# Performance work log

Hardware: AMD Instinct MI355X
Metric: run time of the kernel (lower is better)

## Reference

```python
import math
import jax, jax.numpy as jnp
import numpy as np

IN_DIM, OUT_DIM, NUM_BASIS = 128, 64, 8
EPS = 1e-5

def _periods():
    # periods[i,j,g] = i*(out_dim*num_basis) + j*num_basis + g + 2
    i = jnp.arange(OUT_DIM)[:, None, None]
    j = jnp.arange(OUT_DIM)[None, :, None]
    g = jnp.arange(NUM_BASIS)[None, None, :]
    return (i * (OUT_DIM * NUM_BASIS) + j * NUM_BASIS + g + 2).astype(jnp.float32)

def setup_inputs() -> dict:
    key = jax.random.key(0)
    k1, k2, k3, k4 = jax.random.split(key, 4)
    x = jax.random.normal(k1, (2, 512, IN_DIM), dtype=jnp.float32)
    positions = jnp.arange(512, dtype=jnp.int32)
    M = jax.random.uniform(k2, (OUT_DIM, IN_DIM), minval=-0.5, maxval=0.5, dtype=jnp.float32)
    P = jax.random.uniform(k3, (OUT_DIM, OUT_DIM, NUM_BASIS), minval=-0.1, maxval=0.1, dtype=jnp.float32)
    gamma = jnp.ones((OUT_DIM,), dtype=jnp.float32)
    beta = jnp.zeros((OUT_DIM,), dtype=jnp.float32)
    Wres = jax.random.uniform(k4, (OUT_DIM, IN_DIM), minval=-0.1, maxval=0.1, dtype=jnp.float32)
    return {"x": x, "positions": positions, "M": M, "P": P, "gamma": gamma, "beta": beta, "Wres": Wres}

def reference(x, positions, M, P, gamma, beta, Wres):
    # x: (b, s, in), M: (out, in)
    x_trans = jnp.einsum('bsc,oc->bso', x, M)
    mu = jnp.mean(x_trans, axis=-1, keepdims=True)
    var = jnp.mean(jnp.square(x_trans - mu), axis=-1, keepdims=True)
    x_trans = (x_trans - mu) * jax.lax.rsqrt(var + EPS) * gamma + beta
    # phi[s,i,j,g] = cos(2*pi*k_s / periods[i,j,g])
    k = positions.astype(jnp.float32)[:, None, None, None]
    phi = jnp.cos(2.0 * math.pi * k / _periods())  # (s, out, out, nb)
    # Nk[b,s,i] = sum_{j,g} P[i,j,g] * x_trans[b,s,j] * phi[s,i,j,g]
    W = jnp.einsum('sijg,ijg->sij', phi, P)  # (s, out, out)
    Nk = jnp.einsum('bsj,sij->bsi', x_trans, W)
    residual = jnp.einsum('bsc,oc->bso', x, Wres)  # separate residual proj (in!=out)
    return Nk + residual
```

## Files before the change

kernel.cpp:

```cpp
#include <hip/hip_runtime.h>
#include <hip/hip_bf16.h>

#define IN_DIM    128
#define OUT_DIM   64
#define NUM_BASIS 8
#define SEQ       512
#define BATCH     2
#define EPS       1e-5f
#define SX        2

__global__ __launch_bounds__(512) void fused_layerts_kernel(
    const float* __restrict__ x,
    const float* __restrict__ M,
    const float* __restrict__ Wres,
    const float* __restrict__ gamma,
    const float* __restrict__ beta,
    const float* __restrict__ P,
    const int*   __restrict__ positions,
    float* __restrict__ out)
{
    const int s0  = blockIdx.x * SX;
    const int tid = threadIdx.x;

    __shared__ float xs [SX][BATCH][IN_DIM];
    __shared__ float xts[SX][BATCH][OUT_DIM];
    __shared__ float rs [SX][BATCH][OUT_DIM];
    __shared__ float pm [2][SX * BATCH][OUT_DIM];
    __shared__ float pr [2][SX * BATCH][OUT_DIM];
    __shared__ float part[8][SX][BATCH][OUT_DIM];

    {
        const int row = tid >> 7;
        const int c   = tid & 127;
        const int b   = row & 1;
        const int sl  = row >> 1;
        xs[sl][b][c] = x[((size_t)b * SEQ + (s0 + sl)) * IN_DIM + c];
    }
    const float k0 = (float)positions[s0];
    const float k1 = (float)positions[s0 + 1];
    __syncthreads();

    {
        const int o    = tid & 63;
        const int r    = (tid >> 6) & 3;
        const int half = tid >> 8;
        const int b    = r & 1;
        const int sl   = r >> 1;

        const float4* x4 = reinterpret_cast<const float4*>(&xs[sl][b][half * 64]);
        const float4* m4 = reinterpret_cast<const float4*>(M    + (size_t)o * IN_DIM + half * 64);
        const float4* w4 = reinterpret_cast<const float4*>(Wres + (size_t)o * IN_DIM + half * 64);

        float macc0 = 0.f, macc1 = 0.f, racc0 = 0.f, racc1 = 0.f;
#pragma unroll
        for (int c = 0; c < 16; c += 2) {
            float4 xv0 = x4[c],     mv0 = m4[c],     wv0 = w4[c];
            float4 xv1 = x4[c + 1], mv1 = m4[c + 1], wv1 = w4[c + 1];
            macc0 += xv0.x * mv0.x + xv0.y * mv0.y + xv0.z * mv0.z + xv0.w * mv0.w;
            racc0 += xv0.x * wv0.x + xv0.y * wv0.y + xv0.z * wv0.z + xv0.w * wv0.w;
            macc1 += xv1.x * mv1.x + xv1.y * mv1.y + xv1.z * mv1.z + xv1.w * mv1.w;
            racc1 += xv1.x * wv1.x + xv1.y * wv1.y + xv1.z * wv1.z + xv1.w * wv1.w;
        }
        pm[half][r][o] = macc0 + macc1;
        pr[half][r][o] = racc0 + racc1;
    }
    __syncthreads();

    if (tid < SX * BATCH * OUT_DIM) {
        const int o  = tid & 63;
        const int r  = tid >> 6;
        const int b  = r & 1;
        const int sl = r >> 1;

        const float macc = pm[0][r][o] + pm[1][r][o];
        const float racc = pr[0][r][o] + pr[1][r][o];

        float ssum = macc;
#pragma unroll
        for (int off = 32; off > 0; off >>= 1) ssum += __shfl_xor(ssum, off);
        const float mu = ssum * (1.0f / OUT_DIM);

        const float d = macc - mu;
        float v = d * d;
#pragma unroll
        for (int off = 32; off > 0; off >>= 1) v += __shfl_xor(v, off);
        const float var = v * (1.0f / OUT_DIM);

        xts[sl][b][o] = d * rsqrtf(var + EPS) * gamma[o] + beta[o];
        rs [sl][b][o] = racc;
    }
    __syncthreads();

    const int i   = tid & 63;
    const int grp = tid >> 6;

    float nk00 = 0.f, nk01 = 0.f, nk10 = 0.f, nk11 = 0.f;

#pragma unroll
    for (int jj = 0; jj < 8; ++jj) {
        const int j    = grp * 8 + jj;
        const int base = (i * OUT_DIM + j) * NUM_BASIS;
        const float4* Pp = reinterpret_cast<const float4*>(P + base);
        const float4 p0 = Pp[0];
        const float4 p1 = Pp[1];
        const float basef = (float)(base + 2);

        const float pv[8] = {p0.x, p0.y, p0.z, p0.w, p1.x, p1.y, p1.z, p1.w};
        float w0 = 0.f, w1 = 0.f;
#pragma unroll
        for (int g = 0; g < NUM_BASIS; ++g) {
            const float period = basef + (float)g;
            const float inv = __builtin_amdgcn_rcpf(period);
            float t0 = __builtin_amdgcn_fractf(k0 * inv);
            float t1 = __builtin_amdgcn_fractf(k1 * inv);
            w0 += pv[g] * __builtin_amdgcn_cosf(t0);
            w1 += pv[g] * __builtin_amdgcn_cosf(t1);
        }
        nk00 += xts[0][0][j] * w0;
        nk01 += xts[0][1][j] * w0;
        nk10 += xts[1][0][j] * w1;
        nk11 += xts[1][1][j] * w1;
    }

    part[grp][0][0][i] = nk00;
    part[grp][0][1][i] = nk01;
    part[grp][1][0][i] = nk10;
    part[grp][1][1][i] = nk11;
    __syncthreads();

    if (tid < SX * BATCH * OUT_DIM) {
        const int o  = tid & 63;
        const int r  = tid >> 6;
        const int b  = r & 1;
        const int sl = r >> 1;

        float sum = 0.f;
#pragma unroll
        for (int gg = 0; gg < 8; ++gg) sum += part[gg][sl][b][o];

        const size_t idx = ((size_t)b * SEQ + (s0 + sl)) * OUT_DIM + o;
        out[idx] = sum + rs[sl][b][o];
    }
}

extern "C" void kernel_launch(void* const* d_in, const int* in_sizes, int n_in,
                              void* d_out, int out_size, void* d_ws, size_t ws_size,
                              hipStream_t stream)
{
    const float* x         = (const float*)d_in[0];
    const int*   positions = (const int*)d_in[1];
    const float* M         = (const float*)d_in[2];
    const float* P         = (const float*)d_in[3];
    const float* gamma     = (const float*)d_in[4];
    const float* beta      = (const float*)d_in[5];
    const float* Wres      = (const float*)d_in[6];
    float* out = (float*)d_out;

    hipLaunchKernelGGL(fused_layerts_kernel, dim3(SEQ / SX), dim3(512), 0, stream,
                       x, M, Wres, gamma, beta, P, positions, out);
}
```

Before: 18.13 us.

## Warp-specialize: overlap projection/layernorm waves with cosine basis waves via LDS flag

Splits the block into two groups of four waves. The first group computes the input projection, residual and layernorm directly from global memory, with no shared staging and no split-K. The second group computes the cosine-weighted W rows (16 j each) at the same time, then spins on a workgroup-scope atomic flag before combining with the normalized activations. This removes three block-wide barriers and overlaps the transcendental work with the GEMV. In exchange, each cosine wave does twice the work, holds more registers, and spin-waits.

```diff
diff --git a/kernel.cpp b/kernel.cpp
--- a/kernel.cpp
+++ b/kernel.cpp
@@ -19,61 +19,45 @@
     const int*   __restrict__ positions,
     float* __restrict__ out)
 {
-    const int s0  = blockIdx.x * SX;
-    const int tid = threadIdx.x;
+    const int s0   = blockIdx.x * SX;
+    const int tid  = threadIdx.x;
+    const int lane = tid & 63;
+    const int wv   = tid >> 6;
 
-    __shared__ float xs [SX][BATCH][IN_DIM];
     __shared__ float xts[SX][BATCH][OUT_DIM];
     __shared__ float rs [SX][BATCH][OUT_DIM];
-    __shared__ float pm [2][SX * BATCH][OUT_DIM];
-    __shared__ float pr [2][SX * BATCH][OUT_DIM];
-    __shared__ float part[8][SX][BATCH][OUT_DIM];
+    __shared__ float part[4][SX][BATCH][OUT_DIM];
+    __shared__ int   ready;
 
-    {
-        const int row = tid >> 7;
-        const int c   = tid & 127;
-        const int b   = row & 1;
-        const int sl  = row >> 1;
-        xs[sl][b][c] = x[((size_t)b * SEQ + (s0 + sl)) * IN_DIM + c];
-    }
+    if (tid == 0) ready = 0;
+    __syncthreads();
+
     const float k0 = (float)positions[s0];
     const float k1 = (float)positions[s0 + 1];
-    __syncthreads();
 
-    {
-        const int o    = tid & 63;
-        const int r    = (tid >> 6) & 3;
-        const int half = tid >> 8;
-        const int b    = r & 1;
-        const int sl   = r >> 1;
+    if (wv < 4) {
+        const int r  = wv;
+        const int b  = r & 1;
+        const int sl = r >> 1;
+        const int o  = lane;
 
-        const float4* x4 = reinterpret_cast<const float4*>(&xs[sl][b][half * 64]);
-        const float4* m4 = reinterpret_cast<const float4*>(M    + (size_t)o * IN_DIM + half * 64);
-        const float4* w4 = reinterpret_cast<const float4*>(Wres + (size_t)o * IN_DIM + half * 64);
+        const float4* x4 = reinterpret_cast<const float4*>(
+            x + ((size_t)b * SEQ + (s0 + sl)) * IN_DIM);
+        const float4* m4 = reinterpret_cast<const float4*>(M    + (size_t)o * IN_DIM);
+        const float4* w4 = reinterpret_cast<const float4*>(Wres + (size_t)o * IN_DIM);
 
-        float macc0 = 0.f, macc1 = 0.f, racc0 = 0.f, racc1 = 0.f;
+        float ma = 0.f, mb = 0.f, ra = 0.f, rb = 0.f;
 #pragma unroll
-        for (int c = 0; c < 16; c += 2) {
+        for (int c = 0; c < 32; c += 2) {
             float4 xv0 = x4[c],     mv0 = m4[c],     wv0 = w4[c];
             float4 xv1 = x4[c + 1], mv1 = m4[c + 1], wv1 = w4[c + 1];
-            macc0 += xv0.x * mv0.x + xv0.y * mv0.y + xv0.z * mv0.z + xv0.w * mv0.w;
-            racc0 += xv0.x * wv0.x + xv0.y * wv0.y + xv0.z * wv0.z + xv0.w * wv0.w;
-            macc1 += xv1.x * mv1.x + xv1.y * mv1.y + xv1.z * mv1.z + xv1.w * mv1.w;
-            racc1 += xv1.x * wv1.x + xv1.y * wv1.y + xv1.z * wv1.z + xv1.w * wv1.w;
+            ma += xv0.x * mv0.x + xv0.y * mv0.y + xv0.z * mv0.z + xv0.w * mv0.w;
+            ra += xv0.x * wv0.x + xv0.y * wv0.y + xv0.z * wv0.z + xv0.w * wv0.w;
+            mb += xv1.x * mv1.x + xv1.y * mv1.y + xv1.z * mv1.z + xv1.w * mv1.w;
+            rb += xv1.x * wv1.x + xv1.y * wv1.y + xv1.z * wv1.z + xv1.w * wv1.w;
         }
-        pm[half][r][o] = macc0 + macc1;
-        pr[half][r][o] = racc0 + racc1;
-    }
-    __syncthreads();
-
-    if (tid < SX * BATCH * OUT_DIM) {
-        const int o  = tid & 63;
-        const int r  = tid >> 6;
-        const int b  = r & 1;
-        const int sl = r >> 1;
-
-        const float macc = pm[0][r][o] + pm[1][r][o];
-        const float racc = pr[0][r][o] + pr[1][r][o];
+        const float macc = ma + mb;
+        const float racc = ra + rb;
 
         float ssum = macc;
 #pragma unroll
@@ -88,44 +72,57 @@
 
         xts[sl][b][o] = d * rsqrtf(var + EPS) * gamma[o] + beta[o];
         rs [sl][b][o] = racc;
-    }
-    __syncthreads();
 
-    const int i   = tid & 63;
-    const int grp = tid >> 6;
+        __threadfence_block();
+        if (lane == 0)
+            __hip_atomic_fetch_add(&ready, 1, __ATOMIC_RELEASE,
+                                   __HIP_MEMORY_SCOPE_WORKGROUP);
+    } else {
+        const int g = wv - 4;
+        const int i = lane;
 
-    float nk00 = 0.f, nk01 = 0.f, nk10 = 0.f, nk11 = 0.f;
+        float w0[16], w1[16];
+#pragma unroll
+        for (int jj = 0; jj < 16; ++jj) {
+            const int j    = g * 16 + jj;
+            const int base = (i * OUT_DIM + j) * NUM_BASIS;
+            const float4* Pp = reinterpret_cast<const float4*>(P + base);
+            const float4 p0 = Pp[0];
+            const float4 p1 = Pp[1];
+            const float basef = (float)(base + 2);
 
+            const float pv[8] = {p0.x, p0.y, p0.z, p0.w, p1.x, p1.y, p1.z, p1.w};
+            float a0 = 0.f, a1 = 0.f;
 #pragma unroll
-    for (int jj = 0; jj < 8; ++jj) {
-        const int j    = grp * 8 + jj;
-        const int base = (i * OUT_DIM + j) * NUM_BASIS;
-        const float4* Pp = reinterpret_cast<const float4*>(P + base);
-        const float4 p0 = Pp[0];
-        const float4 p1 = Pp[1];
-        const float basef = (float)(base + 2);
+            for (int gg = 0; gg < NUM_BASIS; ++gg) {
+                const float inv = __builtin_amdgcn_rcpf(basef + (float)gg);
+                a0 += pv[gg] * __builtin_amdgcn_cosf(__builtin_amdgcn_fractf(k0 * inv));
+                a1 += pv[gg] * __builtin_amdgcn_cosf(__builtin_amdgcn_fractf(k1 * inv));
+            }
+            w0[jj] = a0;
+            w1[jj] = a1;
+        }
 
-        const float pv[8] = {p0.x, p0.y, p0.z, p0.w, p1.x, p1.y, p1.z, p1.w};
-        float w0 = 0.f, w1 = 0.f;
+        while (__hip_atomic_load(&ready, __ATOMIC_ACQUIRE,
+                                 __HIP_MEMORY_SCOPE_WORKGROUP) < 4) {
+            __builtin_amdgcn_s_sleep(1);
+        }
+
+        float nk00 = 0.f, nk01 = 0.f, nk10 = 0.f, nk11 = 0.f;
 #pragma unroll
-        for (int g = 0; g < NUM_BASIS; ++g) {
-            const float period = basef + (float)g;
-            const float inv = __builtin_amdgcn_rcpf(period);
-            float t0 = __builtin_amdgcn_fractf(k0 * inv);
-            float t1 = __builtin_amdgcn_fractf(k1 * inv);
-            w0 += pv[g] * __builtin_amdgcn_cosf(t0);
-            w1 += pv[g] * __builtin_amdgcn_cosf(t1);
+        for (int jj = 0; jj < 16; ++jj) {
+            const int j = g * 16 + jj;
+            nk00 += xts[0][0][j] * w0[jj];
+            nk01 += xts[0][1][j] * w0[jj];
+            nk10 += xts[1][0][j] * w1[jj];
+            nk11 += xts[1][1][j] * w1[jj];
         }
-        nk00 += xts[0][0][j] * w0;
-        nk01 += xts[0][1][j] * w0;
-        nk10 += xts[1][0][j] * w1;
-        nk11 += xts[1][1][j] * w1;
+        part[g][0][0][i] = nk00;
+        part[g][0][1][i] = nk01;
+        part[g][1][0][i] = nk10;
+        part[g][1][1][i] = nk11;
     }
 
-    part[grp][0][0][i] = nk00;
-    part[grp][0][1][i] = nk01;
-    part[grp][1][0][i] = nk10;
-    part[grp][1][1][i] = nk11;
     __syncthreads();
 
     if (tid < SX * BATCH * OUT_DIM) {
@@ -134,9 +131,8 @@
         const int b  = r & 1;
         const int sl = r >> 1;
 
-        float sum = 0.f;
-#pragma unroll
-        for (int gg = 0; gg < 8; ++gg) sum += part[gg][sl][b][o];
+        const float sum = part[0][sl][b][o] + part[1][sl][b][o] +
+                          part[2][sl][b][o] + part[3][sl][b][o];
 
         const size_t idx = ((size_t)b * SEQ + (s0 + sl)) * OUT_DIM + o;
         out[idx] = sum + rs[sl][b][o];
```

After: 22.08 us. 21.8% more time.
